# Optimization experiments

Hardware: AMD Instinct MI355X
Metric: run time of the kernel (lower is better)

## Reference

```python
import jax, jax.numpy as jnp
import numpy as np

B, L, C, H = 4, 2048, 1024, 16
D = C // H
MAX_SCALE_MUL = float(np.log(100.0))
EPS = 1e-12


def setup_inputs() -> dict:
    key = jax.random.key(0)
    ks = jax.random.split(key, 7)
    return {
        "x": jax.random.normal(ks[0], (B, L, C), dtype=jnp.float32),
        "W_qkv": jax.random.normal(ks[1], (3 * C, C), dtype=jnp.float32) * (C ** -0.5),
        "q_bias": jax.random.normal(ks[2], (C,), dtype=jnp.float32) * 0.02,
        "v_bias": jax.random.normal(ks[3], (C,), dtype=jnp.float32) * 0.02,
        "scale_mul_log": jnp.full((1, H, 1, 1), np.log(4.0), dtype=jnp.float32),
        "W_proj": jax.random.normal(ks[4], (C, C), dtype=jnp.float32) * (C ** -0.5),
        "b_proj": jax.random.normal(ks[5], (C,), dtype=jnp.float32) * 0.02,
    }


def reference(x, W_qkv, q_bias, v_bias, scale_mul_log, W_proj, b_proj):
    Bb, Ll, Cc = x.shape
    # fused QKV projection with bias = cat(q_bias, zeros, v_bias)
    bias = jnp.concatenate([q_bias, jnp.zeros_like(q_bias), v_bias])
    qkv = (x @ W_qkv.T + bias).reshape(Bb, Ll, 3, H, D)
    q, k, v = (jnp.transpose(qkv[:, :, i], (0, 2, 1, 3)) for i in range(3))  # [B,H,L,D]
    # L2-norm attention: normalize q,k; learned per-head scale on q (clamped)
    scale_mul = jnp.exp(jnp.minimum(scale_mul_log, MAX_SCALE_MUL))  # [1,H,1,1]
    q = q / jnp.maximum(jnp.linalg.norm(q, axis=-1, keepdims=True), EPS) * scale_mul
    k = k / jnp.maximum(jnp.linalg.norm(k, axis=-1, keepdims=True), EPS)
    # SDPA with scale=1 (attn_l2_norm path), no mask, no dropout (eval)
    scores = jnp.einsum("bhqd,bhkd->bhqk", q, k)
    attn = jax.nn.softmax(scores, axis=-1)
    out = jnp.einsum("bhqk,bhkd->bhqd", attn, v)
    out = jnp.transpose(out, (0, 2, 1, 3)).reshape(Bb, Ll, Cc)
    return out @ W_proj.T + b_proj
```

## Files before the change

### kernel.cpp

```cpp
#include <hip/hip_runtime.h>
#include <hip/hip_bf16.h>


typedef __attribute__((ext_vector_type(8))) short bf16x8;
typedef __attribute__((ext_vector_type(16))) float f32x16;

#define MAXLOG 4.60517018598809f
#define LOG2E  1.4426950408889634f

__device__ __forceinline__ float bf2f(unsigned short u) {
    union { unsigned int i; float f; } v; v.i = ((unsigned int)u) << 16; return v.f;
}
__device__ __forceinline__ unsigned short f2bf(float f) {
    union { float f; unsigned int i; } v; v.f = f;
    unsigned int x = v.i;
    return (unsigned short)((x + 0x7FFFu + ((x >> 16) & 1u)) >> 16);
}
__device__ __forceinline__ unsigned fbits(float f) {
    union { float f; unsigned u; } v; v.f = f; return v.u;
}
__device__ __forceinline__ bf16x8 pack8(const float* __restrict__ p) {
    float4 a = *(const float4*)p;
    float4 b = *(const float4*)(p + 4);
    bf16x8 r;
    r[0] = (short)f2bf(a.x); r[1] = (short)f2bf(a.y);
    r[2] = (short)f2bf(a.z); r[3] = (short)f2bf(a.w);
    r[4] = (short)f2bf(b.x); r[5] = (short)f2bf(b.y);
    r[6] = (short)f2bf(b.z); r[7] = (short)f2bf(b.w);
    return r;
}
__device__ __forceinline__ void gload_lds16(const void* g, void* l) {
    __builtin_amdgcn_global_load_lds((const __attribute__((address_space(1))) void*)g,
                                     (__attribute__((address_space(3))) void*)l, 16, 0, 0);
}

__global__ __launch_bounds__(256) void k_prep(
    const float* __restrict__ x, const float* __restrict__ Wqkv,
    const float* __restrict__ Wp, const float* __restrict__ qbia,
    const float* __restrict__ vbia,
    unsigned short* __restrict__ xb, unsigned short* __restrict__ Wqkvb,
    unsigned short* __restrict__ Wpb, float* __restrict__ bias3)
{
    int i = blockIdx.x * 256 + threadIdx.x;
    if (i < 1048576) {
        *(bf16x8*)&xb[(long)i * 8] = pack8(&x[(long)i * 8]);
    } else if (i < 1441792) {
        int j = i - 1048576;
        *(bf16x8*)&Wqkvb[(long)j * 8] = pack8(&Wqkv[(long)j * 8]);
    } else if (i < 1572864) {
        int j = i - 1441792;
        *(bf16x8*)&Wpb[(long)j * 8] = pack8(&Wp[(long)j * 8]);
    } else if (i < 1573248) {
        int j = (i - 1572864) * 8;
        for (int u = 0; u < 8; ++u) {
            int n = j + u;
            float v = 0.0f;
            if (n < 1024) v = qbia[n];
            else if (n >= 2048) v = vbia[n - 2048];
            bias3[n] = v;
        }
    }
}

template<bool OUT_F32>
__global__ __launch_bounds__(256) void k_gemm_lds(
    const unsigned short* __restrict__ A, const unsigned short* __restrict__ Bh,
    const float* __restrict__ bias, void* __restrict__ Cp, int N, int K)
{
    __shared__ unsigned short As[128 * 32];
    __shared__ unsigned short Bs[128 * 32];
    const int t = threadIdx.x, wave = t >> 6, lane = t & 63;
    const int m32 = lane & 31, half = lane >> 5;
    const int bm = blockIdx.x * 128, bn = blockIdx.y * 128;
    const int wr = (wave >> 1) * 64, wc = (wave & 1) * 64;
    f32x16 acc[2][2] = {};

    const int srow = lane >> 2;
    const int scol = (((lane & 3) ^ ((lane >> 3) & 3))) * 8;
    const int c0 = wave * 2, c1 = wave * 2 + 1;
    const long ga0 = (long)(bm + c0 * 16 + srow) * K + scol;
    const long ga1 = (long)(bm + c1 * 16 + srow) * K + scol;
    const long gb0 = (long)(bn + c0 * 16 + srow) * K + scol;
    const long gb1 = (long)(bn + c1 * 16 + srow) * K + scol;

    const int swz = (m32 >> 1) & 3;

    for (int kt = 0; kt < K; kt += 32) {
        __syncthreads();
        gload_lds16(&A[ga0 + kt], &As[c0 * 512]);
        gload_lds16(&A[ga1 + kt], &As[c1 * 512]);
        gload_lds16(&Bh[gb0 + kt], &Bs[c0 * 512]);
        gload_lds16(&Bh[gb1 + kt], &Bs[c1 * 512]);
        __syncthreads();
        bf16x8 af[2][2], bfr[2][2];
        for (int mt = 0; mt < 2; ++mt)
            for (int f = 0; f < 2; ++f)
                af[mt][f] = *(const bf16x8*)&As[(wr + mt * 32 + m32) * 32 +
                                                (((f * 2 + half) ^ swz) * 8)];
        for (int nt = 0; nt < 2; ++nt)
            for (int f = 0; f < 2; ++f)
                bfr[nt][f] = *(const bf16x8*)&Bs[(wc + nt * 32 + m32) * 32 +
                                                 (((f * 2 + half) ^ swz) * 8)];
        for (int f = 0; f < 2; ++f)
            for (int mt = 0; mt < 2; ++mt)
                for (int nt = 0; nt < 2; ++nt)
                    acc[mt][nt] = __builtin_amdgcn_mfma_f32_32x32x16_bf16(
                        af[mt][f], bfr[nt][f], acc[mt][nt], 0, 0, 0);
    }
    for (int mt = 0; mt < 2; ++mt)
        for (int nt = 0; nt < 2; ++nt) {
            int gn = bn + wc + nt * 32 + m32;
            float bv = bias[gn];
            for (int r = 0; r < 16; ++r) {
                int gm = bm + wr + mt * 32 + (r & 3) + 8 * (r >> 2) + 4 * half;
                float val = acc[mt][nt][r] + bv;
                if (OUT_F32) ((float*)Cp)[(long)gm * N + gn] = val;
                else ((unsigned short*)Cp)[(long)gm * N + gn] = f2bf(val);
            }
        }
}

__global__ __launch_bounds__(256) void k_prep_kv(
    const unsigned short* __restrict__ qkv, unsigned short* __restrict__ kb,
    unsigned short* __restrict__ vT)
{
    __shared__ unsigned short Vsh[64 * 72];
    const int t = threadIdx.x;
    const int bh = blockIdx.y, l0 = blockIdx.x * 64;
    const int h = bh & 15, b = bh >> 4;
    const int ll = t >> 2, c16 = (t & 3) * 16;
    const long rowbase = (long)(b * 2048 + l0 + ll) * 3072;

    {
        bf16x8 k0 = *(const bf16x8*)&qkv[rowbase + 1024 + h * 64 + c16];
        bf16x8 k1 = *(const bf16x8*)&qkv[rowbase + 1024 + h * 64 + c16 + 8];
        float e[16]; float ss = 0.f;
        for (int j = 0; j < 8; ++j) { e[j]     = bf2f((unsigned short)k0[j]); ss += e[j] * e[j]; }
        for (int j = 0; j < 8; ++j) { e[8 + j] = bf2f((unsigned short)k1[j]); ss += e[8 + j] * e[8 + j]; }
        ss += __shfl_xor(ss, 1, 64);
        ss += __shfl_xor(ss, 2, 64);
        float rs = 1.0f / fmaxf(sqrtf(ss), 1e-12f);
        bf16x8 o0, o1;
        for (int j = 0; j < 8; ++j) o0[j] = (short)f2bf(e[j] * rs);
        for (int j = 0; j < 8; ++j) o1[j] = (short)f2bf(e[8 + j] * rs);
        long dst = ((long)bh * 2048 + l0 + ll) * 64 + c16;
        *(bf16x8*)&kb[dst]     = o0;
        *(bf16x8*)&kb[dst + 8] = o1;
    }
    *(bf16x8*)&Vsh[ll * 72 + c16]     = *(const bf16x8*)&qkv[rowbase + 2048 + h * 64 + c16];
    *(bf16x8*)&Vsh[ll * 72 + c16 + 8] = *(const bf16x8*)&qkv[rowbase + 2048 + h * 64 + c16 + 8];
    __syncthreads();
    const int d = t >> 2, ls = (t & 3) * 16;
    unsigned short tmp[16];
    for (int j = 0; j < 16; ++j) tmp[j] = Vsh[(ls + j) * 72 + d];
    long dst = (long)(bh * 64 + d) * 2048 + l0 + ls;
    *(bf16x8*)&vT[dst]     = *(bf16x8*)&tmp[0];
    *(bf16x8*)&vT[dst + 8] = *(bf16x8*)&tmp[8];
}

__global__ __launch_bounds__(256, 2) void k_attn32(
    const unsigned short* __restrict__ qkv, const unsigned short* __restrict__ kb,
    const unsigned short* __restrict__ vT, const float* __restrict__ sml,
    unsigned short* __restrict__ attn)
{
    __shared__ unsigned short Ks[2][64 * 72];
    __shared__ unsigned short Vs[2][64 * 72];
    const int t = threadIdx.x, wave = t >> 6, lane = t & 63;
    const int m32 = lane & 31, half = lane >> 5;
    const int wg = blockIdx.x;
    const int logical = (wg & 7) * 64 + (wg >> 3);
    const int bh = logical >> 3, qblk = logical & 7;
    const int h = bh & 15, b = bh >> 4;
    const int q0 = qblk * 256 + wave * 64;
    const float scale = __expf(fminf(sml[h], MAXLOG));
    const float c2 = scale * LOG2E;

    const int qd = m32 >> 2, lo = qd & 3;
    const int prow = ((((lo == 1) || (lo == 2)) ? (qd ^ 3) : qd) << 2) | (m32 & 3);

    bf16x8 aqA[4], aqB[4];
    {
        long base = (long)(b * 2048 + q0 + m32) * 3072 + h * 64;
        float e[32]; float ss = 0.f;
        for (int f = 0; f < 4; ++f) {
            aqA[f] = *(const bf16x8*)&qkv[base + f * 16 + half * 8];
            for (int j = 0; j < 8; ++j) { float x = bf2f((unsigned short)aqA[f][j]); e[f * 8 + j] = x; ss += x * x; }
        }
        ss += __shfl_xor(ss, 32, 64);
        float rs = (scale * LOG2E) / fmaxf(sqrtf(ss), 1e-12f);
        for (int f = 0; f < 4; ++f)
            for (int j = 0; j < 8; ++j) aqA[f][j] = (short)f2bf(e[f * 8 + j] * rs);
    }
    {
        long base = (long)(b * 2048 + q0 + 32 + m32) * 3072 + h * 64;
        float e[32]; float ss = 0.f;
        for (int f = 0; f < 4; ++f) {
            aqB[f] = *(const bf16x8*)&qkv[base + f * 16 + half * 8];
            for (int j = 0; j < 8; ++j) { float x = bf2f((unsigned short)aqB[f][j]); e[f * 8 + j] = x; ss += x * x; }
        }
        ss += __shfl_xor(ss, 32, 64);
        float rs = (scale * LOG2E) / fmaxf(sqrtf(ss), 1e-12f);
        for (int f = 0; f < 4; ++f)
            for (int j = 0; j < 8; ++j) aqB[f][j] = (short)f2bf(e[f * 8 + j] * rs);
    }

    f32x16 oA0 = {}, oA1 = {}, lA = {};
    f32x16 oB0 = {}, oB1 = {}, lB = {};
    bf16x8 ones; for (int i = 0; i < 8; ++i) ones[i] = (short)0x3F80;
    const int sr = t >> 2, sc = (t & 3) * 16;
    const long kbase = (long)bh * 2048 * 64;
    const long vbase = (long)bh * 64 * 2048;

#define LOADT(kt) \
    kpA = *(const bf16x8*)&kb[kbase + (long)((kt) + sr) * 64 + sc];      \
    kpB = *(const bf16x8*)&kb[kbase + (long)((kt) + sr) * 64 + sc + 8];  \
    vpA = *(const bf16x8*)&vT[vbase + (long)sr * 2048 + (kt) + sc];      \
    vpB = *(const bf16x8*)&vT[vbase + (long)sr * 2048 + (kt) + sc + 8];

#define STORET(buf) \
    *(bf16x8*)&Ks[buf][sr * 72 + sc]     = kpA;  \
    *(bf16x8*)&Ks[buf][sr * 72 + sc + 8] = kpB;  \
    *(bf16x8*)&Vs[buf][sr * 72 + sc]     = vpA;  \
    *(bf16x8*)&Vs[buf][sr * 72 + sc + 8] = vpB;

#define SCORE(AQ, AP0, AP1, KF0, KF1, KF2, KF3, SUB) \
    {                                                                                      \
        f32x16 s = {};                                                                     \
        s = __builtin_amdgcn_mfma_f32_32x32x16_bf16(KF0, AQ[0], s, 0, 0, 0);               \
        s = __builtin_amdgcn_mfma_f32_32x32x16_bf16(KF1, AQ[1], s, 0, 0, 0);               \
        s = __builtin_amdgcn_mfma_f32_32x32x16_bf16(KF2, AQ[2], s, 0, 0, 0);               \
        s = __builtin_amdgcn_mfma_f32_32x32x16_bf16(KF3, AQ[3], s, 0, 0, 0);               \
        unsigned pu[16];                                                                   \
        for (int j = 0; j < 16; ++j)                                                       \
            pu[j] = fbits(__builtin_amdgcn_exp2f(s[j] - (SUB)));                           \
        uint4 a0u, a1u;                                                                    \
        a0u.x = __builtin_amdgcn_perm(pu[1],  pu[0],  0x07060302u);                        \
        a0u.y = __builtin_amdgcn_perm(pu[3],  pu[2],  0x07060302u);                        \
        a0u.z = __builtin_amdgcn_perm(pu[5],  pu[4],  0x07060302u);                        \
        a0u.w = __builtin_amdgcn_perm(pu[7],  pu[6],  0x07060302u);                        \
        a1u.x = __builtin_amdgcn_perm(pu[9],  pu[8],  0x07060302u);                        \
        a1u.y = __builtin_amdgcn_perm(pu[11], pu[10], 0x07060302u);                        \
        a1u.z = __builtin_amdgcn_perm(pu[13], pu[12], 0x07060302u);                        \
        a1u.w = __builtin_amdgcn_perm(pu[15], pu[14], 0x07060302u);                        \
        __builtin_memcpy(&AP0, &a0u, 16); __builtin_memcpy(&AP1, &a1u, 16);                \
    }

#define ATTN_STEP(KS, VS, SUB) \
    for (int ktile = 0; ktile < 2; ++ktile) {                                              \
        const unsigned short* krow = &KS[(ktile * 32 + prow) * 72 + half * 8];             \
        bf16x8 kf0 = *(const bf16x8*)&krow[0];                                             \
        bf16x8 kf1 = *(const bf16x8*)&krow[16];                                            \
        bf16x8 kf2 = *(const bf16x8*)&krow[32];                                            \
        bf16x8 kf3 = *(const bf16x8*)&krow[48];                                            \
        bf16x8 apA0, apA1, apB0, apB1;                                                     \
        SCORE(aqA, apA0, apA1, kf0, kf1, kf2, kf3, SUB)                                    \
        SCORE(aqB, apB0, apB1, kf0, kf1, kf2, kf3, SUB)                                    \
        for (int c = 0; c < 2; ++c) {                                                      \
            bf16x8 aA = c ? apA1 : apA0;                                                   \
            bf16x8 aB = c ? apB1 : apB0;                                                   \
            bf16x8 bv0 = *(const bf16x8*)&VS[m32 * 72        + ktile * 32 + c * 16 + half * 8]; \
            bf16x8 bv1 = *(const bf16x8*)&VS[(32 + m32) * 72 + ktile * 32 + c * 16 + half * 8]; \
            oA0 = __builtin_amdgcn_mfma_f32_32x32x16_bf16(aA, bv0, oA0, 0, 0, 0);          \
            oA1 = __builtin_amdgcn_mfma_f32_32x32x16_bf16(aA, bv1, oA1, 0, 0, 0);          \
            lA  = __builtin_amdgcn_mfma_f32_32x32x16_bf16(aA, ones, lA, 0, 0, 0);          \
            oB0 = __builtin_amdgcn_mfma_f32_32x32x16_bf16(aB, bv0, oB0, 0, 0, 0);          \
            oB1 = __builtin_amdgcn_mfma_f32_32x32x16_bf16(aB, bv1, oB1, 0, 0, 0);          \
            lB  = __builtin_amdgcn_mfma_f32_32x32x16_bf16(aB, ones, lB, 0, 0, 0);          \
        }                                                                                  \
    }

#define KLOOP(SUB) \
    for (int kt = 0; kt < 2048; kt += 128) {                 \
        LOADT(kt + 64)                                       \
        ATTN_STEP(Ks[0], Vs[0], SUB)                         \
        STORET(1)                                            \
        __syncthreads();                                     \
        const bool more = (kt + 128) < 2048;                 \
        if (more) { LOADT(kt + 128) }                        \
        ATTN_STEP(Ks[1], Vs[1], SUB)                         \
        if (more) {                                          \
            STORET(0)                                        \
            __syncthreads();                                 \
        }                                                    \
    }

    bf16x8 kpA, kpB, vpA, vpB;
    LOADT(0)
    STORET(0)
    __syncthreads();

    if (c2 < 30.0f) {
        KLOOP(0.0f)
    } else {
        KLOOP(c2)
    }
#undef LOADT
#undef STORET
#undef SCORE
#undef ATTN_STEP
#undef KLOOP

    for (int r = 0; r < 16; ++r) {
        int m = (r & 3) + 8 * (r >> 2) + 4 * half;
        float invA = 1.0f / lA[r];
        long dstA = (long)(b * 2048 + q0 + m) * 1024 + h * 64;
        attn[dstA + m32]      = f2bf(oA0[r] * invA);
        attn[dstA + 32 + m32] = f2bf(oA1[r] * invA);
        float invB = 1.0f / lB[r];
        long dstB = (long)(b * 2048 + q0 + 32 + m) * 1024 + h * 64;
        attn[dstB + m32]      = f2bf(oB0[r] * invB);
        attn[dstB + 32 + m32] = f2bf(oB1[r] * invB);
    }
}

extern "C" void kernel_launch(void* const* d_in, const int* in_sizes, int n_in,
                              void* d_out, int out_size, void* d_ws, size_t ws_size,
                              hipStream_t stream) {
    const float* x    = (const float*)d_in[0];
    const float* Wqkv = (const float*)d_in[1];
    const float* qbia = (const float*)d_in[2];
    const float* vbia = (const float*)d_in[3];
    const float* sml  = (const float*)d_in[4];
    const float* Wp   = (const float*)d_in[5];
    const float* bp   = (const float*)d_in[6];

    char* ws = (char*)d_ws;
    unsigned short* qkv   = (unsigned short*)ws;
    unsigned short* kbuf  = (unsigned short*)(ws + 50331648);
    unsigned short* Wqkvb = kbuf;
    unsigned short* vT    = (unsigned short*)(ws + 67108864);
    unsigned short* xb    = vT;
    unsigned short* attnb = (unsigned short*)(ws + 83886080);
    float*          bias3 = (float*)(ws + 100663296);
    unsigned short* Wpb   = (unsigned short*)(ws + 100679680);
    float*          out   = (float*)d_out;

    hipLaunchKernelGGL(k_prep, dim3(6146), dim3(256), 0, stream,
                       x, Wqkv, Wp, qbia, vbia, xb, Wqkvb, Wpb, bias3);
    hipLaunchKernelGGL((k_gemm_lds<false>), dim3(64, 24), dim3(256), 0, stream,
                       xb, Wqkvb, bias3, (void*)qkv, 3072, 1024);
    hipLaunchKernelGGL(k_prep_kv, dim3(32, 64), dim3(256), 0, stream, qkv, kbuf, vT);
    hipLaunchKernelGGL(k_attn32, dim3(512), dim3(256), 0, stream, qkv, kbuf, vT, sml, attnb);
    hipLaunchKernelGGL((k_gemm_lds<true>), dim3(64, 8), dim3(256), 0, stream,
                       attnb, Wpb, bp, (void*)out, 1024, 1024);
}
```

Before: 275.0 us.

## Fuse K L2-normalization into QKV GEMM epilogue and double-buffer GEMM LDS tiles

The QKV GEMM epilogue now L2-normalizes the K columns per head in place, using a cross-lane shuffle reduction over the 64-wide head. This removes the separate normalized-K buffer and its pass in the prep kernel, and attention now reads K directly from the strided qkv rows. The GEMM main loop also double-buffers its LDS tiles, issuing the next tile's loads before the current tile's MFMAs, which halves the syncs per iteration and doubles LDS use. The trade-off is that attention K loads now use a 3072-element stride, making them less contiguous.

```diff
diff --git a/kernel.cpp b/kernel.cpp
--- a/kernel.cpp
+++ b/kernel.cpp
@@ -62,13 +62,13 @@
     }
 }
 
-template<bool OUT_F32>
+template<bool OUT_F32, bool KNORM>
 __global__ __launch_bounds__(256) void k_gemm_lds(
     const unsigned short* __restrict__ A, const unsigned short* __restrict__ Bh,
     const float* __restrict__ bias, void* __restrict__ Cp, int N, int K)
 {
-    __shared__ unsigned short As[128 * 32];
-    __shared__ unsigned short Bs[128 * 32];
+    __shared__ unsigned short As[2][128 * 32];
+    __shared__ unsigned short Bs[2][128 * 32];
     const int t = threadIdx.x, wave = t >> 6, lane = t & 63;
     const int m32 = lane & 31, half = lane >> 5;
     const int bm = blockIdx.x * 128, bn = blockIdx.y * 128;
@@ -85,44 +85,68 @@
 
     const int swz = (m32 >> 1) & 3;
 
+    gload_lds16(&A[ga0], &As[0][c0 * 512]);
+    gload_lds16(&A[ga1], &As[0][c1 * 512]);
+    gload_lds16(&Bh[gb0], &Bs[0][c0 * 512]);
+    gload_lds16(&Bh[gb1], &Bs[0][c1 * 512]);
+    __syncthreads();
+
+    int cur = 0;
     for (int kt = 0; kt < K; kt += 32) {
-        __syncthreads();
-        gload_lds16(&A[ga0 + kt], &As[c0 * 512]);
-        gload_lds16(&A[ga1 + kt], &As[c1 * 512]);
-        gload_lds16(&Bh[gb0 + kt], &Bs[c0 * 512]);
-        gload_lds16(&Bh[gb1 + kt], &Bs[c1 * 512]);
-        __syncthreads();
+        const int nxt = kt + 32;
+        if (nxt < K) {
+            gload_lds16(&A[ga0 + nxt], &As[cur ^ 1][c0 * 512]);
+            gload_lds16(&A[ga1 + nxt], &As[cur ^ 1][c1 * 512]);
+            gload_lds16(&Bh[gb0 + nxt], &Bs[cur ^ 1][c0 * 512]);
+            gload_lds16(&Bh[gb1 + nxt], &Bs[cur ^ 1][c1 * 512]);
+        }
         bf16x8 af[2][2], bfr[2][2];
         for (int mt = 0; mt < 2; ++mt)
             for (int f = 0; f < 2; ++f)
-                af[mt][f] = *(const bf16x8*)&As[(wr + mt * 32 + m32) * 32 +
-                                                (((f * 2 + half) ^ swz) * 8)];
+                af[mt][f] = *(const bf16x8*)&As[cur][(wr + mt * 32 + m32) * 32 +
+                                                    (((f * 2 + half) ^ swz) * 8)];
         for (int nt = 0; nt < 2; ++nt)
             for (int f = 0; f < 2; ++f)
-                bfr[nt][f] = *(const bf16x8*)&Bs[(wc + nt * 32 + m32) * 32 +
-                                                 (((f * 2 + half) ^ swz) * 8)];
+                bfr[nt][f] = *(const bf16x8*)&Bs[cur][(wc + nt * 32 + m32) * 32 +
+                                                     (((f * 2 + half) ^ swz) * 8)];
         for (int f = 0; f < 2; ++f)
             for (int mt = 0; mt < 2; ++mt)
                 for (int nt = 0; nt < 2; ++nt)
                     acc[mt][nt] = __builtin_amdgcn_mfma_f32_32x32x16_bf16(
                         af[mt][f], bfr[nt][f], acc[mt][nt], 0, 0, 0);
-    }
+        __syncthreads();
+        cur ^= 1;
+    }
+
+    const bool isk = KNORM && (bn >= 1024) && (bn < 2048);
+    const float bv0 = bias[bn + wc + m32];
+    const float bv1 = bias[bn + wc + 32 + m32];
     for (int mt = 0; mt < 2; ++mt)
-        for (int nt = 0; nt < 2; ++nt) {
-            int gn = bn + wc + nt * 32 + m32;
-            float bv = bias[gn];
-            for (int r = 0; r < 16; ++r) {
-                int gm = bm + wr + mt * 32 + (r & 3) + 8 * (r >> 2) + 4 * half;
-                float val = acc[mt][nt][r] + bv;
+        for (int r = 0; r < 16; ++r) {
+            int gm = bm + wr + mt * 32 + (r & 3) + 8 * (r >> 2) + 4 * half;
+            float inv = 1.0f;
+            if (isk) {
+                float ss = acc[mt][0][r] * acc[mt][0][r]
+                         + acc[mt][1][r] * acc[mt][1][r];
+                ss += __shfl_xor(ss, 1, 64);
+                ss += __shfl_xor(ss, 2, 64);
+                ss += __shfl_xor(ss, 4, 64);
+                ss += __shfl_xor(ss, 8, 64);
+                ss += __shfl_xor(ss, 16, 64);
+                inv = 1.0f / fmaxf(sqrtf(ss), 1e-12f);
+            }
+            for (int nt = 0; nt < 2; ++nt) {
+                int gn = bn + wc + nt * 32 + m32;
+                float val = acc[mt][nt][r] + (nt ? bv1 : bv0);
+                if (isk) val *= inv;
                 if (OUT_F32) ((float*)Cp)[(long)gm * N + gn] = val;
                 else ((unsigned short*)Cp)[(long)gm * N + gn] = f2bf(val);
             }
         }
 }
 
-__global__ __launch_bounds__(256) void k_prep_kv(
-    const unsigned short* __restrict__ qkv, unsigned short* __restrict__ kb,
-    unsigned short* __restrict__ vT)
+__global__ __launch_bounds__(256) void k_prep_v(
+    const unsigned short* __restrict__ qkv, unsigned short* __restrict__ vT)
 {
     __shared__ unsigned short Vsh[64 * 72];
     const int t = threadIdx.x;
@@ -131,22 +155,6 @@
     const int ll = t >> 2, c16 = (t & 3) * 16;
     const long rowbase = (long)(b * 2048 + l0 + ll) * 3072;
 
-    {
-        bf16x8 k0 = *(const bf16x8*)&qkv[rowbase + 1024 + h * 64 + c16];
-        bf16x8 k1 = *(const bf16x8*)&qkv[rowbase + 1024 + h * 64 + c16 + 8];
-        float e[16]; float ss = 0.f;
-        for (int j = 0; j < 8; ++j) { e[j]     = bf2f((unsigned short)k0[j]); ss += e[j] * e[j]; }
-        for (int j = 0; j < 8; ++j) { e[8 + j] = bf2f((unsigned short)k1[j]); ss += e[8 + j] * e[8 + j]; }
-        ss += __shfl_xor(ss, 1, 64);
-        ss += __shfl_xor(ss, 2, 64);
-        float rs = 1.0f / fmaxf(sqrtf(ss), 1e-12f);
-        bf16x8 o0, o1;
-        for (int j = 0; j < 8; ++j) o0[j] = (short)f2bf(e[j] * rs);
-        for (int j = 0; j < 8; ++j) o1[j] = (short)f2bf(e[8 + j] * rs);
-        long dst = ((long)bh * 2048 + l0 + ll) * 64 + c16;
-        *(bf16x8*)&kb[dst]     = o0;
-        *(bf16x8*)&kb[dst + 8] = o1;
-    }
     *(bf16x8*)&Vsh[ll * 72 + c16]     = *(const bf16x8*)&qkv[rowbase + 2048 + h * 64 + c16];
     *(bf16x8*)&Vsh[ll * 72 + c16 + 8] = *(const bf16x8*)&qkv[rowbase + 2048 + h * 64 + c16 + 8];
     __syncthreads();
@@ -159,7 +167,7 @@
 }
 
 __global__ __launch_bounds__(256, 2) void k_attn32(
-    const unsigned short* __restrict__ qkv, const unsigned short* __restrict__ kb,
+    const unsigned short* __restrict__ qkv,
     const unsigned short* __restrict__ vT, const float* __restrict__ sml,
     unsigned short* __restrict__ attn)
 {
@@ -208,13 +216,13 @@
     f32x16 oB0 = {}, oB1 = {}, lB = {};
     bf16x8 ones; for (int i = 0; i < 8; ++i) ones[i] = (short)0x3F80;
     const int sr = t >> 2, sc = (t & 3) * 16;
-    const long kbase = (long)bh * 2048 * 64;
+    const long kqrow = (long)(b * 2048) * 3072 + 1024 + h * 64;
     const long vbase = (long)bh * 64 * 2048;
 
 #define LOADT(kt) \
-    kpA = *(const bf16x8*)&kb[kbase + (long)((kt) + sr) * 64 + sc];      \
-    kpB = *(const bf16x8*)&kb[kbase + (long)((kt) + sr) * 64 + sc + 8];  \
-    vpA = *(const bf16x8*)&vT[vbase + (long)sr * 2048 + (kt) + sc];      \
+    kpA = *(const bf16x8*)&qkv[kqrow + (long)((kt) + sr) * 3072 + sc];      \
+    kpB = *(const bf16x8*)&qkv[kqrow + (long)((kt) + sr) * 3072 + sc + 8];  \
+    vpA = *(const bf16x8*)&vT[vbase + (long)sr * 2048 + (kt) + sc];         \
     vpB = *(const bf16x8*)&vT[vbase + (long)sr * 2048 + (kt) + sc + 8];
 
 #define STORET(buf) \
@@ -326,8 +334,7 @@
 
     char* ws = (char*)d_ws;
     unsigned short* qkv   = (unsigned short*)ws;
-    unsigned short* kbuf  = (unsigned short*)(ws + 50331648);
-    unsigned short* Wqkvb = kbuf;
+    unsigned short* Wqkvb = (unsigned short*)(ws + 50331648);
     unsigned short* vT    = (unsigned short*)(ws + 67108864);
     unsigned short* xb    = vT;
     unsigned short* attnb = (unsigned short*)(ws + 83886080);
@@ -337,10 +344,10 @@
 
     hipLaunchKernelGGL(k_prep, dim3(6146), dim3(256), 0, stream,
                        x, Wqkv, Wp, qbia, vbia, xb, Wqkvb, Wpb, bias3);
-    hipLaunchKernelGGL((k_gemm_lds<false>), dim3(64, 24), dim3(256), 0, stream,
+    hipLaunchKernelGGL((k_gemm_lds<false, true>), dim3(64, 24), dim3(256), 0, stream,
                        xb, Wqkvb, bias3, (void*)qkv, 3072, 1024);
-    hipLaunchKernelGGL(k_prep_kv, dim3(32, 64), dim3(256), 0, stream, qkv, kbuf, vT);
-    hipLaunchKernelGGL(k_attn32, dim3(512), dim3(256), 0, stream, qkv, kbuf, vT, sml, attnb);
-    hipLaunchKernelGGL((k_gemm_lds<true>), dim3(64, 8), dim3(256), 0, stream,
+    hipLaunchKernelGGL(k_prep_v, dim3(32, 64), dim3(256), 0, stream, qkv, vT);
+    hipLaunchKernelGGL(k_attn32, dim3(512), dim3(256), 0, stream, qkv, vT, sml, attnb);
+    hipLaunchKernelGGL((k_gemm_lds<true, false>), dim3(64, 8), dim3(256), 0, stream,
                        attnb, Wpb, bp, (void*)out, 1024, 1024);
 }
```

Measured after the change: 279.7 us. No clear change (+1.7%).

## Fuse K L2-normalization into larger-tile QKV GEMM epilogue, read K directly in attention

Applied to the files above, without the earlier changes.

Adds a new QKV GEMM kernel with 256x128 tiles. For column blocks covering K, its epilogue L2-normalizes each 64-wide head row with cross-lane shuffles before storing bf16. The K-normalization part of the prep kernel is dropped, so that pass now only transposes V. Attention reads normalized K straight from the strided qkv buffer instead of a packed K buffer. This saves one read and one write of K and changes the GEMM tiling, at the cost of strided K loads in attention and extra shuffles in the GEMM epilogue.

```diff
diff --git a/kernel.cpp b/kernel.cpp
--- a/kernel.cpp
+++ b/kernel.cpp
@@ -62,6 +62,87 @@
     }
 }
 
+template<bool KNORM>
+__global__ __launch_bounds__(256, 2) void k_gemm256(
+    const unsigned short* __restrict__ A, const unsigned short* __restrict__ Bh,
+    const float* __restrict__ bias, unsigned short* __restrict__ Cp,
+    int N, int K)
+{
+    __shared__ unsigned short As[256 * 32];
+    __shared__ unsigned short Bs[128 * 32];
+    const int t = threadIdx.x, wave = t >> 6, lane = t & 63;
+    const int m32 = lane & 31, half = lane >> 5;
+    const int bm = blockIdx.x * 256, bn = blockIdx.y * 128;
+    f32x16 acc[2][4] = {};
+
+    const int srow = lane >> 2;
+    const int scol = (((lane & 3) ^ ((lane >> 3) & 3))) * 8;
+    long gA[4], gB[2];
+    for (int i = 0; i < 4; ++i)
+        gA[i] = (long)(bm + (wave * 4 + i) * 16 + srow) * K + scol;
+    for (int i = 0; i < 2; ++i)
+        gB[i] = (long)(bn + (wave * 2 + i) * 16 + srow) * K + scol;
+
+    const int swz = (m32 >> 1) & 3;
+
+    for (int kt = 0; kt < K; kt += 32) {
+        __syncthreads();
+        for (int i = 0; i < 4; ++i)
+            gload_lds16(&A[gA[i] + kt], &As[(wave * 4 + i) * 512]);
+        for (int i = 0; i < 2; ++i)
+            gload_lds16(&Bh[gB[i] + kt], &Bs[(wave * 2 + i) * 512]);
+        __syncthreads();
+        bf16x8 af[2][2], bfr[4][2];
+        for (int mt = 0; mt < 2; ++mt)
+            for (int f = 0; f < 2; ++f)
+                af[mt][f] = *(const bf16x8*)&As[(wave * 64 + mt * 32 + m32) * 32 +
+                                                (((f * 2 + half) ^ swz) * 8)];
+        for (int nt = 0; nt < 4; ++nt)
+            for (int f = 0; f < 2; ++f)
+                bfr[nt][f] = *(const bf16x8*)&Bs[(nt * 32 + m32) * 32 +
+                                                 (((f * 2 + half) ^ swz) * 8)];
+        for (int f = 0; f < 2; ++f)
+            for (int mt = 0; mt < 2; ++mt)
+                for (int nt = 0; nt < 4; ++nt)
+                    acc[mt][nt] = __builtin_amdgcn_mfma_f32_32x32x16_bf16(
+                        af[mt][f], bfr[nt][f], acc[mt][nt], 0, 0, 0);
+    }
+
+    const bool isk = KNORM && (bn >= 1024) && (bn < 2048);
+    float bv[4];
+    for (int nt = 0; nt < 4; ++nt) bv[nt] = bias[bn + nt * 32 + m32];
+    for (int mt = 0; mt < 2; ++mt)
+        for (int r = 0; r < 16; ++r) {
+            int gm = bm + wave * 64 + mt * 32 + (r & 3) + 8 * (r >> 2) + 4 * half;
+            float v0 = acc[mt][0][r] + bv[0];
+            float v1 = acc[mt][1][r] + bv[1];
+            float v2 = acc[mt][2][r] + bv[2];
+            float v3 = acc[mt][3][r] + bv[3];
+            if (isk) {
+                float sa = v0 * v0 + v1 * v1;
+                sa += __shfl_xor(sa, 1, 64);
+                sa += __shfl_xor(sa, 2, 64);
+                sa += __shfl_xor(sa, 4, 64);
+                sa += __shfl_xor(sa, 8, 64);
+                sa += __shfl_xor(sa, 16, 64);
+                float sb = v2 * v2 + v3 * v3;
+                sb += __shfl_xor(sb, 1, 64);
+                sb += __shfl_xor(sb, 2, 64);
+                sb += __shfl_xor(sb, 4, 64);
+                sb += __shfl_xor(sb, 8, 64);
+                sb += __shfl_xor(sb, 16, 64);
+                float ia = 1.0f / fmaxf(sqrtf(sa), 1e-12f);
+                float ib = 1.0f / fmaxf(sqrtf(sb), 1e-12f);
+                v0 *= ia; v1 *= ia; v2 *= ib; v3 *= ib;
+            }
+            long rowb = (long)gm * N + bn + m32;
+            Cp[rowb]      = f2bf(v0);
+            Cp[rowb + 32] = f2bf(v1);
+            Cp[rowb + 64] = f2bf(v2);
+            Cp[rowb + 96] = f2bf(v3);
+        }
+}
+
 template<bool OUT_F32>
 __global__ __launch_bounds__(256) void k_gemm_lds(
     const unsigned short* __restrict__ A, const unsigned short* __restrict__ Bh,
@@ -120,9 +201,8 @@
         }
 }
 
-__global__ __launch_bounds__(256) void k_prep_kv(
-    const unsigned short* __restrict__ qkv, unsigned short* __restrict__ kb,
-    unsigned short* __restrict__ vT)
+__global__ __launch_bounds__(256) void k_prep_v(
+    const unsigned short* __restrict__ qkv, unsigned short* __restrict__ vT)
 {
     __shared__ unsigned short Vsh[64 * 72];
     const int t = threadIdx.x;
@@ -131,22 +211,6 @@
     const int ll = t >> 2, c16 = (t & 3) * 16;
     const long rowbase = (long)(b * 2048 + l0 + ll) * 3072;
 
-    {
-        bf16x8 k0 = *(const bf16x8*)&qkv[rowbase + 1024 + h * 64 + c16];
-        bf16x8 k1 = *(const bf16x8*)&qkv[rowbase + 1024 + h * 64 + c16 + 8];
-        float e[16]; float ss = 0.f;
-        for (int j = 0; j < 8; ++j) { e[j]     = bf2f((unsigned short)k0[j]); ss += e[j] * e[j]; }
-        for (int j = 0; j < 8; ++j) { e[8 + j] = bf2f((unsigned short)k1[j]); ss += e[8 + j] * e[8 + j]; }
-        ss += __shfl_xor(ss, 1, 64);
-        ss += __shfl_xor(ss, 2, 64);
-        float rs = 1.0f / fmaxf(sqrtf(ss), 1e-12f);
-        bf16x8 o0, o1;
-        for (int j = 0; j < 8; ++j) o0[j] = (short)f2bf(e[j] * rs);
-        for (int j = 0; j < 8; ++j) o1[j] = (short)f2bf(e[8 + j] * rs);
-        long dst = ((long)bh * 2048 + l0 + ll) * 64 + c16;
-        *(bf16x8*)&kb[dst]     = o0;
-        *(bf16x8*)&kb[dst + 8] = o1;
-    }
     *(bf16x8*)&Vsh[ll * 72 + c16]     = *(const bf16x8*)&qkv[rowbase + 2048 + h * 64 + c16];
     *(bf16x8*)&Vsh[ll * 72 + c16 + 8] = *(const bf16x8*)&qkv[rowbase + 2048 + h * 64 + c16 + 8];
     __syncthreads();
@@ -159,7 +223,7 @@
 }
 
 __global__ __launch_bounds__(256, 2) void k_attn32(
-    const unsigned short* __restrict__ qkv, const unsigned short* __restrict__ kb,
+    const unsigned short* __restrict__ qkv,
     const unsigned short* __restrict__ vT, const float* __restrict__ sml,
     unsigned short* __restrict__ attn)
 {
@@ -208,13 +272,13 @@
     f32x16 oB0 = {}, oB1 = {}, lB = {};
     bf16x8 ones; for (int i = 0; i < 8; ++i) ones[i] = (short)0x3F80;
     const int sr = t >> 2, sc = (t & 3) * 16;
-    const long kbase = (long)bh * 2048 * 64;
+    const long kqrow = (long)(b * 2048) * 3072 + 1024 + h * 64;
     const long vbase = (long)bh * 64 * 2048;
 
 #define LOADT(kt) \
-    kpA = *(const bf16x8*)&kb[kbase + (long)((kt) + sr) * 64 + sc];      \
-    kpB = *(const bf16x8*)&kb[kbase + (long)((kt) + sr) * 64 + sc + 8];  \
-    vpA = *(const bf16x8*)&vT[vbase + (long)sr * 2048 + (kt) + sc];      \
+    kpA = *(const bf16x8*)&qkv[kqrow + (long)((kt) + sr) * 3072 + sc];      \
+    kpB = *(const bf16x8*)&qkv[kqrow + (long)((kt) + sr) * 3072 + sc + 8];  \
+    vpA = *(const bf16x8*)&vT[vbase + (long)sr * 2048 + (kt) + sc];         \
     vpB = *(const bf16x8*)&vT[vbase + (long)sr * 2048 + (kt) + sc + 8];
 
 #define STORET(buf) \
@@ -326,8 +390,7 @@
 
     char* ws = (char*)d_ws;
     unsigned short* qkv   = (unsigned short*)ws;
-    unsigned short* kbuf  = (unsigned short*)(ws + 50331648);
-    unsigned short* Wqkvb = kbuf;
+    unsigned short* Wqkvb = (unsigned short*)(ws + 50331648);
     unsigned short* vT    = (unsigned short*)(ws + 67108864);
     unsigned short* xb    = vT;
     unsigned short* attnb = (unsigned short*)(ws + 83886080);
@@ -337,10 +400,10 @@
 
     hipLaunchKernelGGL(k_prep, dim3(6146), dim3(256), 0, stream,
                        x, Wqkv, Wp, qbia, vbia, xb, Wqkvb, Wpb, bias3);
-    hipLaunchKernelGGL((k_gemm_lds<false>), dim3(64, 24), dim3(256), 0, stream,
-                       xb, Wqkvb, bias3, (void*)qkv, 3072, 1024);
-    hipLaunchKernelGGL(k_prep_kv, dim3(32, 64), dim3(256), 0, stream, qkv, kbuf, vT);
-    hipLaunchKernelGGL(k_attn32, dim3(512), dim3(256), 0, stream, qkv, kbuf, vT, sml, attnb);
+    hipLaunchKernelGGL((k_gemm256<true>), dim3(32, 24), dim3(256), 0, stream,
+                       xb, Wqkvb, bias3, qkv, 3072, 1024);
+    hipLaunchKernelGGL(k_prep_v, dim3(32, 64), dim3(256), 0, stream, qkv, vT);
+    hipLaunchKernelGGL(k_attn32, dim3(512), dim3(256), 0, stream, qkv, vT, sml, attnb);
     hipLaunchKernelGGL((k_gemm_lds<true>), dim3(64, 8), dim3(256), 0, stream,
                        attnb, Wpb, bp, (void*)out, 1024, 1024);
 }
```

Measured after the change: 280.7 us. +2.1%, slower.
